# Kernel tuning notes

Measured on AMD Instinct MI355X. Metric: run time of the kernel, lower is better.

Reference implementation:

```python
import jax, jax.numpy as jnp
import numpy as np

D_IN = 1024
D_OUT = 1024


def setup_inputs() -> dict:
    key = jax.random.key(0)
    kx, kq, kk, kv = jax.random.split(key, 4)
    s = 1.0 / np.sqrt(D_IN)
    x = jax.random.normal(kx, (2, 4096, D_IN), dtype=jnp.float32)
    # nn.Linear weights: shape [d_out, d_in], y = x @ W.T (no bias)
    W_query = jax.random.normal(kq, (D_OUT, D_IN), dtype=jnp.float32) * s
    W_key = jax.random.normal(kk, (D_OUT, D_IN), dtype=jnp.float32) * s
    W_value = jax.random.normal(kv, (D_OUT, D_IN), dtype=jnp.float32) * s
    return {"x": x, "W_query": W_query, "W_key": W_key, "W_value": W_value}


def reference(x, W_query, W_key, W_value):
    # QKV projections: [b, n, d_in] @ [d_in, d_out]
    q = jnp.einsum('bnd,od->bno', x, W_query)
    k = jnp.einsum('bnd,od->bno', x, W_key)
    v = jnp.einsum('bnd,od->bno', x, W_value)
    d_k = k.shape[-1]
    scores = jnp.einsum('bqo,bko->bqk', q, k) / jnp.sqrt(jnp.asarray(d_k, x.dtype))
    # NOTE: source applies no causal mask despite the class name
    attn = jax.nn.softmax(scores, axis=-1)
    return jnp.einsum('bqk,bko->bqo', attn, v)
```

## Files before the change

kernel.cpp:

```cpp
#include <hip/hip_runtime.h>
#include <hip/hip_bf16.h>
#include <hip/hip_fp16.h>
#include <stdint.h>

typedef __bf16 bf16_t;
typedef __bf16 bf16x8 __attribute__((ext_vector_type(8)));
typedef float f32x4 __attribute__((ext_vector_type(4)));

typedef __attribute__((address_space(1))) void gv_t;
typedef __attribute__((address_space(3))) void lv_t;

__device__ inline unsigned short f2bf_bits(float f) {
  uint32_t u = __float_as_uint(f);
  u += 0x7FFFu + ((u >> 16) & 1u);
  return (unsigned short)(u >> 16);
}
__device__ inline bf16_t f2bf(float f) {
  unsigned short h = f2bf_bits(f);
  return __builtin_bit_cast(bf16_t, h);
}

__device__ inline void storeC(float* p, float v) { *p = v; }
__device__ inline void storeC(bf16_t* p, float v) { *p = f2bf(v); }
__device__ inline void storeC(__half* p, float v) { *p = __float2half(v); }

__global__ __launch_bounds__(256)
void convert_all(const float* __restrict__ x, const float* __restrict__ wq,
                 const float* __restrict__ wk, const float* __restrict__ wv,
                 bf16_t* __restrict__ xb, bf16_t* __restrict__ wqkb,
                 bf16_t* __restrict__ wvb)
{
  const int64_t NX = 8192LL * 1024, NW = 1024LL * 1024;
  const int64_t total4 = (NX + 3 * NW) >> 2;
  for (int64_t i = (int64_t)blockIdx.x * blockDim.x + threadIdx.x; i < total4;
       i += (int64_t)gridDim.x * blockDim.x) {
    int64_t e = i << 2;
    const float* src; bf16_t* dst; int64_t off;
    if (e < NX)               { src = x;  dst = xb;         off = e; }
    else if (e < NX + NW)     { src = wq; dst = wqkb;       off = e - NX; }
    else if (e < NX + 2 * NW) { src = wk; dst = wqkb + NW;  off = e - NX - NW; }
    else                      { src = wv; dst = wvb;        off = e - NX - 2 * NW; }
    float4 f = *(const float4*)(src + off);
    uint32_t lo = ((uint32_t)f2bf_bits(f.y) << 16) | f2bf_bits(f.x);
    uint32_t hi = ((uint32_t)f2bf_bits(f.w) << 16) | f2bf_bits(f.z);
    *(uint2*)(dst + off) = make_uint2(lo, hi);
  }
}

template <typename OUT_T, typename OUT2_T>
__global__ __launch_bounds__(256, 2)
void gemm128(const bf16_t* __restrict__ A, const bf16_t* __restrict__ B,
             OUT_T* __restrict__ C0, OUT2_T* __restrict__ C1,
             int K, int lda, int ldb, int ldc,
             int64_t b_batch_stride, int bm_per_batch,
             int64_t za_off, int64_t zb_off)
{
  __shared__ bf16_t As[2][128][64];
  __shared__ bf16_t Bs[2][128][64];

  const int tid  = threadIdx.x;
  const int wid  = tid >> 6;
  const int lane = tid & 63;
  const int wm = wid >> 1;
  const int wn = wid & 1;
  const int64_t bm = blockIdx.x;
  const int64_t bn = blockIdx.y;
  const int z = blockIdx.z;

  const bf16_t* Ap = A + (int64_t)z * za_off;
  const bf16_t* Bp = B + (bm / bm_per_batch) * b_batch_stride
                       + (int64_t)z * zb_off;

  const int srow  = tid >> 3;
  const int sslot = (tid & 7) ^ (srow & 7);
  const int64_t lda64 = lda, ldb64 = ldb;
  const bf16_t* Ag = Ap + (bm * 128 + srow) * lda64 + sslot * 8;
  const bf16_t* Bg = Bp + (bn * 128 + srow) * ldb64 + sslot * 8;

  auto stageA = [&](int buf, int t, int q) {
    const bf16_t* src = Ag + (int64_t)(q * 32) * lda64 + t * 64;
    char* dst = (char*)&As[buf][0][0] + (q * 32 + wid * 8) * 128;
    __builtin_amdgcn_global_load_lds((const gv_t*)src, (lv_t*)dst, 16, 0, 0);
  };
  auto stageB = [&](int buf, int t, int q) {
    const bf16_t* src = Bg + (int64_t)(q * 32) * ldb64 + t * 64;
    char* dst = (char*)&Bs[buf][0][0] + (q * 32 + wid * 8) * 128;
    __builtin_amdgcn_global_load_lds((const gv_t*)src, (lv_t*)dst, 16, 0, 0);
  };

  const int frow   = lane & 15;
  const int fcol16 = lane >> 4;
  const int xorv   = (lane & 7) << 4;
  const int ck0 = (fcol16 * 16) ^ xorv;
  const int ck1 = (64 + fcol16 * 16) ^ xorv;
  const int arowb = (wm * 64 + frow) * 128;
  const int browb = (wn * 64 + frow) * 128;

  f32x4 acc[4][4];
  #pragma unroll
  for (int m = 0; m < 4; m++)
    #pragma unroll
    for (int n = 0; n < 4; n++) acc[m][n] = f32x4{0.f, 0.f, 0.f, 0.f};

  const int NT = K >> 6;

  stageA(0, 0, 0); stageA(0, 0, 1); stageA(0, 0, 2); stageA(0, 0, 3);
  stageB(0, 0, 0); stageB(0, 0, 1); stageB(0, 0, 2); stageB(0, 0, 3);
  asm volatile("s_waitcnt vmcnt(0)" ::: "memory");
  __builtin_amdgcn_s_barrier();
  __builtin_amdgcn_sched_barrier(0);

  bf16x8 a[4][2], bb[4][2];

  for (int g = 0; g < NT; ++g) {
    const int buf = g & 1;
    const char* lA = (const char*)&As[buf][0][0];
    const char* lB = (const char*)&Bs[buf][0][0];

    #pragma unroll
    for (int m = 0; m < 4; m++)
      a[m][0] = *(const bf16x8*)(lA + arowb + m * 2048 + ck0);
    #pragma unroll
    for (int n = 0; n < 4; n++)
      bb[n][0] = *(const bf16x8*)(lB + browb + n * 2048 + ck0);
    #pragma unroll
    for (int m = 0; m < 4; m++)
      a[m][1] = *(const bf16x8*)(lA + arowb + m * 2048 + ck1);
    #pragma unroll
    for (int n = 0; n < 4; n++)
      bb[n][1] = *(const bf16x8*)(lB + browb + n * 2048 + ck1);

    if (g + 1 < NT) {
      stageA(buf ^ 1, g + 1, 0); stageA(buf ^ 1, g + 1, 1);
      stageA(buf ^ 1, g + 1, 2); stageA(buf ^ 1, g + 1, 3);
      stageB(buf ^ 1, g + 1, 0); stageB(buf ^ 1, g + 1, 1);
      stageB(buf ^ 1, g + 1, 2); stageB(buf ^ 1, g + 1, 3);
    }

    __builtin_amdgcn_s_setprio(1);
    #pragma unroll
    for (int k = 0; k < 2; k++)
      #pragma unroll
      for (int m = 0; m < 4; m++)
        #pragma unroll
        for (int n = 0; n < 4; n++)
          acc[m][n] = __builtin_amdgcn_mfma_f32_16x16x32_bf16(
              a[m][k], bb[n][k], acc[m][n], 0, 0, 0);
    __builtin_amdgcn_s_setprio(0);

    asm volatile("s_waitcnt vmcnt(0)" ::: "memory");
    __builtin_amdgcn_s_barrier();
    __builtin_amdgcn_sched_barrier(0);
  }

  const int crow = (lane >> 4) * 4;
  const int ccol = lane & 15;
  if (z == 0) {
    #pragma unroll
    for (int m = 0; m < 4; m++)
      #pragma unroll
      for (int n = 0; n < 4; n++)
        #pragma unroll
        for (int j = 0; j < 4; j++) {
          int64_t row = bm * 128 + wm * 64 + m * 16 + crow + j;
          int64_t col = bn * 128 + wn * 64 + n * 16 + ccol;
          storeC(&C0[row * (int64_t)ldc + col], acc[m][n][j]);
        }
  } else {
    #pragma unroll
    for (int m = 0; m < 4; m++)
      #pragma unroll
      for (int n = 0; n < 4; n++)
        #pragma unroll
        for (int j = 0; j < 4; j++) {
          int64_t row = bm * 128 + wm * 64 + m * 16 + crow + j;
          int64_t col = bn * 128 + wn * 64 + n * 16 + ccol;
          storeC(&C1[row * (int64_t)ldc + col], acc[m][n][j]);
        }
  }
}

__global__ __launch_bounds__(256)
void softmax_rows(__half* __restrict__ SP)
{
  const int64_t row = blockIdx.x;
  __half* s = SP + row * 4096;
  bf16_t* p = (bf16_t*)s;
  const int tid = threadIdx.x;
  const float scale = 0.03125f;

  float v[16];
  float vmax = -3.4e38f;
  #pragma unroll
  for (int i = 0; i < 4; i++) {
    uint2 raw = *(const uint2*)(s + i * 1024 + tid * 4);
    __half2 h01 = __builtin_bit_cast(__half2, raw.x);
    __half2 h23 = __builtin_bit_cast(__half2, raw.y);
    float2 f01 = __half22float2(h01);
    float2 f23 = __half22float2(h23);
    v[i * 4 + 0] = f01.x * scale;
    v[i * 4 + 1] = f01.y * scale;
    v[i * 4 + 2] = f23.x * scale;
    v[i * 4 + 3] = f23.y * scale;
    vmax = fmaxf(vmax, fmaxf(fmaxf(v[i*4+0], v[i*4+1]),
                             fmaxf(v[i*4+2], v[i*4+3])));
  }
  #pragma unroll
  for (int o = 32; o > 0; o >>= 1) vmax = fmaxf(vmax, __shfl_xor(vmax, o));
  __shared__ float redm[4];
  __shared__ float reds[4];
  if ((tid & 63) == 0) redm[tid >> 6] = vmax;
  __syncthreads();
  vmax = fmaxf(fmaxf(redm[0], redm[1]), fmaxf(redm[2], redm[3]));

  float lsum = 0.f;
  #pragma unroll
  for (int i = 0; i < 16; i++) {
    v[i] = __expf(v[i] - vmax);
    lsum += v[i];
  }
  #pragma unroll
  for (int o = 32; o > 0; o >>= 1) lsum += __shfl_xor(lsum, o);
  if ((tid & 63) == 0) reds[tid >> 6] = lsum;
  __syncthreads();
  lsum = (reds[0] + reds[1]) + (reds[2] + reds[3]);
  const float inv = 1.0f / lsum;

  #pragma unroll
  for (int i = 0; i < 4; i++) {
    uint32_t lo = ((uint32_t)f2bf_bits(v[i*4+1] * inv) << 16) | f2bf_bits(v[i*4+0] * inv);
    uint32_t hi = ((uint32_t)f2bf_bits(v[i*4+3] * inv) << 16) | f2bf_bits(v[i*4+2] * inv);
    *(uint2*)(p + i * 1024 + tid * 4) = make_uint2(lo, hi);
  }
}

__global__ __launch_bounds__(256)
void addk_h4(float4* __restrict__ o, const uint2* __restrict__ a, int64_t n4)
{
  for (int64_t i = (int64_t)blockIdx.x * blockDim.x + threadIdx.x; i < n4;
       i += (int64_t)gridDim.x * blockDim.x) {
    float4 x = o[i];
    uint2 raw = a[i];
    __half2 h01 = __builtin_bit_cast(__half2, raw.x);
    __half2 h23 = __builtin_bit_cast(__half2, raw.y);
    float2 f01 = __half22float2(h01);
    float2 f23 = __half22float2(h23);
    x.x += f01.x; x.y += f01.y; x.z += f23.x; x.w += f23.y;
    o[i] = x;
  }
}

extern "C" void kernel_launch(void* const* d_in, const int* in_sizes, int n_in,
                              void* d_out, int out_size, void* d_ws, size_t ws_size,
                              hipStream_t stream) {
  const float* x  = (const float*)d_in[0];
  const float* wq = (const float*)d_in[1];
  const float* wk = (const float*)d_in[2];
  const float* wv = (const float*)d_in[3];
  float* out = (float*)d_out;

  char* ws = (char*)d_ws;
  bf16_t* xb   = (bf16_t*)ws;
  bf16_t* wqkb = (bf16_t*)(ws + (16LL << 20));
  bf16_t* wvb  = (bf16_t*)(ws + (20LL << 20));
  __half* S    = (__half*)ws;
  bf16_t* qk   = (bf16_t*)(ws + (64LL << 20));
  __half* pk16 = (__half*)(ws + (64LL << 20));
  bf16_t* vt   = (bf16_t*)(ws + (96LL << 20));

  const int NO_BATCH = 1 << 30;

  convert_all<<<2048, 256, 0, stream>>>(x, wq, wk, wv, xb, wqkb, wvb);

  gemm128<bf16_t, bf16_t><<<dim3(64, 16, 1), 256, 0, stream>>>(
      xb, wqkb, qk, qk, 1024, 1024, 1024, 2048, 0, NO_BATCH, 0, 0);

  gemm128<bf16_t, bf16_t><<<dim3(8, 64, 1), 256, 0, stream>>>(
      wvb, xb, vt, vt, 1024, 1024, 1024, 8192, 0, NO_BATCH, 0, 0);

  gemm128<__half, __half><<<dim3(64, 32, 1), 256, 0, stream>>>(
      qk, qk + 1024, S, S, 1024, 2048, 2048, 4096, 4096LL * 2048, 32, 0, 0);

  softmax_rows<<<8192, 256, 0, stream>>>(S);

  gemm128<float, __half><<<dim3(64, 8, 2), 256, 0, stream>>>(
      (const bf16_t*)S, vt, out, pk16, 2048, 4096, 8192, 1024,
      4096, 32, 2048, 2048);

  addk_h4<<<2048, 256, 0, stream>>>((float4*)out, (const uint2*)pk16,
                                    8192LL * 1024 / 4);
}
```

Baseline: 247.7 us.

## Add 256x256-tile GEMM kernel and use it for QK, scores and PV GEMMs

Introduces gemm_fat, a 256x256 block-tile GEMM where each wave computes a 128x128 sub-tile with 8x8 MFMA accumulators, double-buffered LDS via global_load_lds with XOR swizzling. Three of the four GEMMs switch to it with grids and per-batch block counts adjusted. Larger tiles raise arithmetic intensity and cut global/LDS traffic per FLOP. The cost is heavy register pressure (256 accumulator floats per thread), 128KB of LDS so only one block per CU, and fewer blocks, which may hurt occupancy and load balance across the 256 CUs.

```diff
diff --git a/kernel.cpp b/kernel.cpp
--- a/kernel.cpp
+++ b/kernel.cpp
@@ -180,6 +180,141 @@
   }
 }
 
+template <typename OUT_T, typename OUT2_T>
+__global__ __launch_bounds__(256, 1)
+void gemm_fat(const bf16_t* __restrict__ A, const bf16_t* __restrict__ B,
+              OUT_T* __restrict__ C0, OUT2_T* __restrict__ C1,
+              int K, int lda, int ldb, int ldc,
+              int64_t b_batch_stride, int bm_per_batch,
+              int64_t za_off, int64_t zb_off)
+{
+  __shared__ bf16_t As[2][256][64];
+  __shared__ bf16_t Bs[2][256][64];
+
+  const int tid  = threadIdx.x;
+  const int wid  = tid >> 6;
+  const int lane = tid & 63;
+  const int wm = wid >> 1;
+  const int wn = wid & 1;
+  const int64_t bm = blockIdx.x;
+  const int64_t bn = blockIdx.y;
+  const int z = blockIdx.z;
+
+  const bf16_t* Ap = A + (int64_t)z * za_off;
+  const bf16_t* Bp = B + (bm / bm_per_batch) * b_batch_stride
+                       + (int64_t)z * zb_off;
+
+  const int srow  = tid >> 3;
+  const int sslot = (tid & 7) ^ (srow & 7);
+  const int64_t lda64 = lda, ldb64 = ldb;
+  const bf16_t* Ag = Ap + (bm * 256 + srow) * lda64 + sslot * 8;
+  const bf16_t* Bg = Bp + (bn * 256 + srow) * ldb64 + sslot * 8;
+
+  auto stageA = [&](int buf, int t, int q) {
+    const bf16_t* src = Ag + (int64_t)(q * 32) * lda64 + t * 64;
+    char* dst = (char*)&As[buf][0][0] + (q * 32 + wid * 8) * 128;
+    __builtin_amdgcn_global_load_lds((const gv_t*)src, (lv_t*)dst, 16, 0, 0);
+  };
+  auto stageB = [&](int buf, int t, int q) {
+    const bf16_t* src = Bg + (int64_t)(q * 32) * ldb64 + t * 64;
+    char* dst = (char*)&Bs[buf][0][0] + (q * 32 + wid * 8) * 128;
+    __builtin_amdgcn_global_load_lds((const gv_t*)src, (lv_t*)dst, 16, 0, 0);
+  };
+
+  const int frow   = lane & 15;
+  const int fcol16 = lane >> 4;
+  const int xorv   = (lane & 7) << 4;
+  const int ck0 = (fcol16 * 16) ^ xorv;
+  const int ck1 = (64 + fcol16 * 16) ^ xorv;
+  const int arowb = (wm * 128 + frow) * 128;
+  const int browb = (wn * 128 + frow) * 128;
+
+  f32x4 acc[8][8];
+  #pragma unroll
+  for (int m = 0; m < 8; m++)
+    #pragma unroll
+    for (int n = 0; n < 8; n++) acc[m][n] = f32x4{0.f, 0.f, 0.f, 0.f};
+
+  const int NT = K >> 6;
+
+  #pragma unroll
+  for (int q = 0; q < 8; q++) stageA(0, 0, q);
+  #pragma unroll
+  for (int q = 0; q < 8; q++) stageB(0, 0, q);
+  asm volatile("s_waitcnt vmcnt(0)" ::: "memory");
+  __builtin_amdgcn_s_barrier();
+  __builtin_amdgcn_sched_barrier(0);
+
+  bf16x8 a[8][2], bb[8][2];
+
+  for (int g = 0; g < NT; ++g) {
+    const int buf = g & 1;
+    const char* lA = (const char*)&As[buf][0][0];
+    const char* lB = (const char*)&Bs[buf][0][0];
+
+    #pragma unroll
+    for (int m = 0; m < 8; m++)
+      a[m][0] = *(const bf16x8*)(lA + arowb + m * 2048 + ck0);
+    #pragma unroll
+    for (int n = 0; n < 8; n++)
+      bb[n][0] = *(const bf16x8*)(lB + browb + n * 2048 + ck0);
+    #pragma unroll
+    for (int m = 0; m < 8; m++)
+      a[m][1] = *(const bf16x8*)(lA + arowb + m * 2048 + ck1);
+    #pragma unroll
+    for (int n = 0; n < 8; n++)
+      bb[n][1] = *(const bf16x8*)(lB + browb + n * 2048 + ck1);
+
+    if (g + 1 < NT) {
+      #pragma unroll
+      for (int q = 0; q < 8; q++) stageA(buf ^ 1, g + 1, q);
+      #pragma unroll
+      for (int q = 0; q < 8; q++) stageB(buf ^ 1, g + 1, q);
+    }
+
+    __builtin_amdgcn_s_setprio(1);
+    #pragma unroll
+    for (int k = 0; k < 2; k++)
+      #pragma unroll
+      for (int m = 0; m < 8; m++)
+        #pragma unroll
+        for (int n = 0; n < 8; n++)
+          acc[m][n] = __builtin_amdgcn_mfma_f32_16x16x32_bf16(
+              a[m][k], bb[n][k], acc[m][n], 0, 0, 0);
+    __builtin_amdgcn_s_setprio(0);
+
+    asm volatile("s_waitcnt vmcnt(0)" ::: "memory");
+    __builtin_amdgcn_s_barrier();
+    __builtin_amdgcn_sched_barrier(0);
+  }
+
+  const int crow = (lane >> 4) * 4;
+  const int ccol = lane & 15;
+  if (z == 0) {
+    #pragma unroll
+    for (int m = 0; m < 8; m++)
+      #pragma unroll
+      for (int n = 0; n < 8; n++)
+        #pragma unroll
+        for (int j = 0; j < 4; j++) {
+          int64_t row = bm * 256 + wm * 128 + m * 16 + crow + j;
+          int64_t col = bn * 256 + wn * 128 + n * 16 + ccol;
+          storeC(&C0[row * (int64_t)ldc + col], acc[m][n][j]);
+        }
+  } else {
+    #pragma unroll
+    for (int m = 0; m < 8; m++)
+      #pragma unroll
+      for (int n = 0; n < 8; n++)
+        #pragma unroll
+        for (int j = 0; j < 4; j++) {
+          int64_t row = bm * 256 + wm * 128 + m * 16 + crow + j;
+          int64_t col = bn * 256 + wn * 128 + n * 16 + ccol;
+          storeC(&C1[row * (int64_t)ldc + col], acc[m][n][j]);
+        }
+  }
+}
+
 __global__ __launch_bounds__(256)
 void softmax_rows(__half* __restrict__ SP)
 {
@@ -272,20 +407,20 @@
 
   convert_all<<<2048, 256, 0, stream>>>(x, wq, wk, wv, xb, wqkb, wvb);
 
-  gemm128<bf16_t, bf16_t><<<dim3(64, 16, 1), 256, 0, stream>>>(
+  gemm_fat<bf16_t, bf16_t><<<dim3(32, 8, 1), 256, 0, stream>>>(
       xb, wqkb, qk, qk, 1024, 1024, 1024, 2048, 0, NO_BATCH, 0, 0);
 
   gemm128<bf16_t, bf16_t><<<dim3(8, 64, 1), 256, 0, stream>>>(
       wvb, xb, vt, vt, 1024, 1024, 1024, 8192, 0, NO_BATCH, 0, 0);
 
-  gemm128<__half, __half><<<dim3(64, 32, 1), 256, 0, stream>>>(
-      qk, qk + 1024, S, S, 1024, 2048, 2048, 4096, 4096LL * 2048, 32, 0, 0);
+  gemm_fat<__half, __half><<<dim3(32, 16, 1), 256, 0, stream>>>(
+      qk, qk + 1024, S, S, 1024, 2048, 2048, 4096, 4096LL * 2048, 16, 0, 0);
 
   softmax_rows<<<8192, 256, 0, stream>>>(S);
 
-  gemm128<float, __half><<<dim3(64, 8, 2), 256, 0, stream>>>(
+  gemm_fat<float, __half><<<dim3(32, 4, 2), 256, 0, stream>>>(
       (const bf16_t*)S, vt, out, pk16, 2048, 4096, 8192, 1024,
-      4096, 32, 2048, 2048);
+      4096, 16, 2048, 2048);
 
   addk_h4<<<2048, 256, 0, stream>>>((float4*)out, (const uint2*)pk16,
                                     8192LL * 1024 / 4);
```

Result: no change. 244.5 us (-1.3%).

## Use 256x128 GEMM tiles with 8 waves and triple-buffered LDS prefetch

Applied to the files above, without the earlier changes.

Turns the GEMM into a 512-thread kernel whose block covers 256x128 outputs, with each wave still computing a 64x64 sub-tile. This raises B-tile reuse per block. LDS staging moves from double to triple buffering with a two-tile-ahead prefetch and a partial vmcnt wait, so global loads overlap more compute. Per-block LDS grows to 144KB, which likely lowers occupancy. The grid also gets fewer, larger blocks, which may cut parallelism for the smaller projection GEMMs.

```diff
diff --git a/kernel.cpp b/kernel.cpp
--- a/kernel.cpp
+++ b/kernel.cpp
@@ -48,15 +48,15 @@
 }
 
 template <typename OUT_T, typename OUT2_T>
-__global__ __launch_bounds__(256, 2)
-void gemm128(const bf16_t* __restrict__ A, const bf16_t* __restrict__ B,
-             OUT_T* __restrict__ C0, OUT2_T* __restrict__ C1,
-             int K, int lda, int ldb, int ldc,
-             int64_t b_batch_stride, int bm_per_batch,
-             int64_t za_off, int64_t zb_off)
+__global__ __launch_bounds__(512, 2)
+void gemm3(const bf16_t* __restrict__ A, const bf16_t* __restrict__ B,
+           OUT_T* __restrict__ C0, OUT2_T* __restrict__ C1,
+           int K, int lda, int ldb, int ldc,
+           int64_t b_batch_stride, int bm_per_batch,
+           int64_t za_off, int64_t zb_off)
 {
-  __shared__ bf16_t As[2][128][64];
-  __shared__ bf16_t Bs[2][128][64];
+  __shared__ bf16_t As[3][256][64];
+  __shared__ bf16_t Bs[3][128][64];
 
   const int tid  = threadIdx.x;
   const int wid  = tid >> 6;
@@ -74,18 +74,23 @@
   const int srow  = tid >> 3;
   const int sslot = (tid & 7) ^ (srow & 7);
   const int64_t lda64 = lda, ldb64 = ldb;
-  const bf16_t* Ag = Ap + (bm * 128 + srow) * lda64 + sslot * 8;
+  const bf16_t* Ag = Ap + (bm * 256 + srow) * lda64 + sslot * 8;
   const bf16_t* Bg = Bp + (bn * 128 + srow) * ldb64 + sslot * 8;
 
   auto stageA = [&](int buf, int t, int q) {
-    const bf16_t* src = Ag + (int64_t)(q * 32) * lda64 + t * 64;
-    char* dst = (char*)&As[buf][0][0] + (q * 32 + wid * 8) * 128;
+    const bf16_t* src = Ag + (int64_t)(q * 64) * lda64 + t * 64;
+    char* dst = (char*)&As[buf][0][0] + (q * 64 + wid * 8) * 128;
     __builtin_amdgcn_global_load_lds((const gv_t*)src, (lv_t*)dst, 16, 0, 0);
   };
   auto stageB = [&](int buf, int t, int q) {
-    const bf16_t* src = Bg + (int64_t)(q * 32) * ldb64 + t * 64;
-    char* dst = (char*)&Bs[buf][0][0] + (q * 32 + wid * 8) * 128;
+    const bf16_t* src = Bg + (int64_t)(q * 64) * ldb64 + t * 64;
+    char* dst = (char*)&Bs[buf][0][0] + (q * 64 + wid * 8) * 128;
     __builtin_amdgcn_global_load_lds((const gv_t*)src, (lv_t*)dst, 16, 0, 0);
+  };
+  auto stageTile = [&](int buf, int t) {
+    stageA(buf, t, 0); stageA(buf, t, 1);
+    stageA(buf, t, 2); stageA(buf, t, 3);
+    stageB(buf, t, 0); stageB(buf, t, 1);
   };
 
   const int frow   = lane & 15;
@@ -104,16 +109,20 @@
 
   const int NT = K >> 6;
 
-  stageA(0, 0, 0); stageA(0, 0, 1); stageA(0, 0, 2); stageA(0, 0, 3);
-  stageB(0, 0, 0); stageB(0, 0, 1); stageB(0, 0, 2); stageB(0, 0, 3);
-  asm volatile("s_waitcnt vmcnt(0)" ::: "memory");
+  stageTile(0, 0);
+  if (1 < NT) {
+    stageTile(1, 1);
+    asm volatile("s_waitcnt vmcnt(6)" ::: "memory");
+  } else {
+    asm volatile("s_waitcnt vmcnt(0)" ::: "memory");
+  }
   __builtin_amdgcn_s_barrier();
   __builtin_amdgcn_sched_barrier(0);
 
   bf16x8 a[4][2], bb[4][2];
 
   for (int g = 0; g < NT; ++g) {
-    const int buf = g & 1;
+    const int buf = g % 3;
     const char* lA = (const char*)&As[buf][0][0];
     const char* lB = (const char*)&Bs[buf][0][0];
 
@@ -130,12 +139,7 @@
     for (int n = 0; n < 4; n++)
       bb[n][1] = *(const bf16x8*)(lB + browb + n * 2048 + ck1);
 
-    if (g + 1 < NT) {
-      stageA(buf ^ 1, g + 1, 0); stageA(buf ^ 1, g + 1, 1);
-      stageA(buf ^ 1, g + 1, 2); stageA(buf ^ 1, g + 1, 3);
-      stageB(buf ^ 1, g + 1, 0); stageB(buf ^ 1, g + 1, 1);
-      stageB(buf ^ 1, g + 1, 2); stageB(buf ^ 1, g + 1, 3);
-    }
+    if (g + 2 < NT) stageTile((g + 2) % 3, g + 2);
 
     __builtin_amdgcn_s_setprio(1);
     #pragma unroll
@@ -148,7 +152,11 @@
               a[m][k], bb[n][k], acc[m][n], 0, 0, 0);
     __builtin_amdgcn_s_setprio(0);
 
-    asm volatile("s_waitcnt vmcnt(0)" ::: "memory");
+    if (g + 2 < NT) {
+      asm volatile("s_waitcnt vmcnt(6)" ::: "memory");
+    } else {
+      asm volatile("s_waitcnt vmcnt(0)" ::: "memory");
+    }
     __builtin_amdgcn_s_barrier();
     __builtin_amdgcn_sched_barrier(0);
   }
@@ -162,7 +170,7 @@
       for (int n = 0; n < 4; n++)
         #pragma unroll
         for (int j = 0; j < 4; j++) {
-          int64_t row = bm * 128 + wm * 64 + m * 16 + crow + j;
+          int64_t row = bm * 256 + wm * 64 + m * 16 + crow + j;
           int64_t col = bn * 128 + wn * 64 + n * 16 + ccol;
           storeC(&C0[row * (int64_t)ldc + col], acc[m][n][j]);
         }
@@ -173,7 +181,7 @@
       for (int n = 0; n < 4; n++)
         #pragma unroll
         for (int j = 0; j < 4; j++) {
-          int64_t row = bm * 128 + wm * 64 + m * 16 + crow + j;
+          int64_t row = bm * 256 + wm * 64 + m * 16 + crow + j;
           int64_t col = bn * 128 + wn * 64 + n * 16 + ccol;
           storeC(&C1[row * (int64_t)ldc + col], acc[m][n][j]);
         }
@@ -272,20 +280,20 @@
 
   convert_all<<<2048, 256, 0, stream>>>(x, wq, wk, wv, xb, wqkb, wvb);
 
-  gemm128<bf16_t, bf16_t><<<dim3(64, 16, 1), 256, 0, stream>>>(
+  gemm3<bf16_t, bf16_t><<<dim3(32, 16, 1), 512, 0, stream>>>(
       xb, wqkb, qk, qk, 1024, 1024, 1024, 2048, 0, NO_BATCH, 0, 0);
 
-  gemm128<bf16_t, bf16_t><<<dim3(8, 64, 1), 256, 0, stream>>>(
+  gemm3<bf16_t, bf16_t><<<dim3(4, 64, 1), 512, 0, stream>>>(
       wvb, xb, vt, vt, 1024, 1024, 1024, 8192, 0, NO_BATCH, 0, 0);
 
-  gemm128<__half, __half><<<dim3(64, 32, 1), 256, 0, stream>>>(
-      qk, qk + 1024, S, S, 1024, 2048, 2048, 4096, 4096LL * 2048, 32, 0, 0);
+  gemm3<__half, __half><<<dim3(32, 32, 1), 512, 0, stream>>>(
+      qk, qk + 1024, S, S, 1024, 2048, 2048, 4096, 4096LL * 2048, 16, 0, 0);
 
   softmax_rows<<<8192, 256, 0, stream>>>(S);
 
-  gemm128<float, __half><<<dim3(64, 8, 2), 256, 0, stream>>>(
+  gemm3<float, __half><<<dim3(32, 8, 2), 512, 0, stream>>>(
       (const bf16_t*)S, vt, out, pk16, 2048, 4096, 8192, 1024,
-      4096, 32, 2048, 2048);
+      4096, 16, 2048, 2048);
 
   addk_h4<<<2048, 256, 0, stream>>>((float4*)out, (const uint2*)pk16,
                                     8192LL * 1024 / 4);
```

Result: no change. 247.1 us (-0.3%).
